# Kernel optimization log

Measured on AMD Instinct MI355X. Metric: run time of the kernel, lower is better.

Reference implementation:

```python
import jax, jax.numpy as jnp
import numpy as np

B, S, H = 2, 2048, 1024
HFF = 4096
E, K = 8, 2

def setup_inputs() -> dict:
    key = jax.random.key(0)
    k1, k2, k3, k4, k5 = jax.random.split(key, 5)
    x = jax.random.normal(k1, (B, S, H), dtype=jnp.float32)
    topk_probs = jax.random.uniform(k2, (B, S, K), dtype=jnp.float32)
    topk_indices = jax.random.randint(k3, (B, S, K), 0, E, dtype=jnp.int64)
    stdv = 1.0 / np.sqrt(H)
    W1 = jax.random.uniform(k4, (E, HFF, H), minval=-stdv, maxval=stdv, dtype=jnp.float32)
    stdv2 = 1.0 / np.sqrt(HFF)
    W2 = jax.random.uniform(k5, (E, H, HFF), minval=-stdv2, maxval=stdv2, dtype=jnp.float32)
    return {"x": x, "topk_probs": topk_probs, "topk_indices": topk_indices, "W1": W1, "W2": W2}

def reference(x, topk_probs, topk_indices, W1, W2):
    # gate[b,s,e] = max_k topk_probs[b,s,k] * (topk_indices[b,s,k]==e)
    # (max over k, matching probs_mask.max(dim=-1) in the torch module)
    e_ids = jnp.arange(E, dtype=topk_indices.dtype)  # [E]
    sel = topk_indices[..., None] == e_ids  # [B,S,K,E]
    gate = jnp.max(jnp.where(sel, topk_probs[..., None], 0.0), axis=2)  # [B,S,E]
    # dense per-expert FFN over all tokens (as the original computes)
    h = jnp.einsum('bsh,efh->ebsf', x, W1)       # [E,B,S,HFF]
    h = jax.nn.gelu(h)
    y = jnp.einsum('ebsf,ehf->ebsh', h, W2)      # [E,B,S,H]
    # probability applied after FFN, masked combine over experts
    out = jnp.einsum('bse,ebsh->bsh', gate, y)   # [B,S,H]
    return out
```

## Files before the change

### kernel.cpp

```cpp
#include <hip/hip_runtime.h>

typedef unsigned short ushort_t;
typedef __attribute__((ext_vector_type(8))) short short8;
typedef __attribute__((ext_vector_type(4))) float f32x4;

#define TOKENS  4096
#define H_DIM   1024
#define HFF_DIM 4096
#define NEXP    8

__device__ __forceinline__ ushort_t f2b(float f) {
    union { float f; unsigned u; } v; v.f = f;
    unsigned r = v.u + 0x7fffu + ((v.u >> 16) & 1u);
    return (ushort_t)(r >> 16);
}

__device__ __forceinline__ float gelu_tanh(float x) {
    float u = 0.7978845608028654f * (x + 0.044715f * x * x * x);
    return 0.5f * x * (1.0f + tanhf(u));
}

__global__ void route_kernel(const float* __restrict__ probs,
                             const int* __restrict__ idx,
                             int* __restrict__ count,
                             int* __restrict__ token_id,
                             float* __restrict__ gate) {
    int t = blockIdx.x * blockDim.x + threadIdx.x;
    if (t >= TOKENS) return;
    int i0 = idx[t * 2 + 0];
    int i1 = idx[t * 2 + 1];
    float p0 = probs[t * 2 + 0];
    float p1 = probs[t * 2 + 1];
    if (i0 == i1) {
        float p = fmaxf(p0, p1);
        int pos = atomicAdd(&count[i0], 1);
        token_id[i0 * TOKENS + pos] = t;
        gate[i0 * TOKENS + pos] = p;
    } else {
        int pos = atomicAdd(&count[i0], 1);
        token_id[i0 * TOKENS + pos] = t;
        gate[i0 * TOKENS + pos] = p0;
        pos = atomicAdd(&count[i1], 1);
        token_id[i1 * TOKENS + pos] = t;
        gate[i1 * TOKENS + pos] = p1;
    }
}

__global__ void prefix_kernel(const int* __restrict__ count, int* __restrict__ offsets) {
    if (threadIdx.x == 0 && blockIdx.x == 0) {
        int acc = 0;
        for (int e = 0; e < NEXP; ++e) { offsets[e] = acc; acc += count[e]; }
        offsets[NEXP] = acc;
    }
}

__global__ __launch_bounds__(256) void gemm1_kernel(
        const float* __restrict__ x, const float* __restrict__ W1,
        const int* __restrict__ count, const int* __restrict__ offsets,
        const int* __restrict__ token_id, ushort_t* __restrict__ h) {
    const int e = blockIdx.z;
    const int cnt = count[e];
    const int mt = blockIdx.y;
    if (mt * 128 >= cnt) return;
    const int nt = blockIdx.x;
    const int base = offsets[e];

    __shared__ __align__(16) ushort_t As[128 * 32];
    __shared__ __align__(16) ushort_t Bs[128 * 32];

    const int tid = threadIdx.x;
    const int srow = tid >> 1;
    const int scol = (tid & 1) << 4;

    int am = mt * 128 + srow;
    int amc = am < cnt ? am : (cnt - 1);
    const int tok = token_id[e * TOKENS + amc];
    const float* aptr = x + (size_t)tok * H_DIM + scol;
    const float* bptr = W1 + (size_t)e * HFF_DIM * H_DIM
                        + (size_t)(nt * 128 + srow) * H_DIM + scol;

    const int lane = tid & 63;
    const int wave = tid >> 6;
    const int wm = (wave >> 1) << 6;
    const int wn = (wave & 1) << 6;
    const int lr = lane & 15;
    const int lq = lane >> 4;

    f32x4 acc[4][4];
#pragma unroll
    for (int mi = 0; mi < 4; ++mi)
#pragma unroll
        for (int ni = 0; ni < 4; ++ni)
            acc[mi][ni] = (f32x4){0.f, 0.f, 0.f, 0.f};

    for (int k0 = 0; k0 < H_DIM; k0 += 32) {
        ushort_t ta[16], tb[16];
        const float4* pa = (const float4*)(aptr + k0);
        const float4* pb = (const float4*)(bptr + k0);
#pragma unroll
        for (int i = 0; i < 4; ++i) {
            float4 va = pa[i];
            ta[i * 4 + 0] = f2b(va.x); ta[i * 4 + 1] = f2b(va.y);
            ta[i * 4 + 2] = f2b(va.z); ta[i * 4 + 3] = f2b(va.w);
            float4 vb = pb[i];
            tb[i * 4 + 0] = f2b(vb.x); tb[i * 4 + 1] = f2b(vb.y);
            tb[i * 4 + 2] = f2b(vb.z); tb[i * 4 + 3] = f2b(vb.w);
        }
        __syncthreads();
        *(short8*)&As[srow * 32 + scol]     = *(short8*)&ta[0];
        *(short8*)&As[srow * 32 + scol + 8] = *(short8*)&ta[8];
        *(short8*)&Bs[srow * 32 + scol]     = *(short8*)&tb[0];
        *(short8*)&Bs[srow * 32 + scol + 8] = *(short8*)&tb[8];
        __syncthreads();

        short8 af[4], bf[4];
#pragma unroll
        for (int mi = 0; mi < 4; ++mi)
            af[mi] = *(const short8*)&As[(wm + mi * 16 + lr) * 32 + lq * 8];
#pragma unroll
        for (int ni = 0; ni < 4; ++ni)
            bf[ni] = *(const short8*)&Bs[(wn + ni * 16 + lr) * 32 + lq * 8];
#pragma unroll
        for (int mi = 0; mi < 4; ++mi)
#pragma unroll
            for (int ni = 0; ni < 4; ++ni)
                acc[mi][ni] = __builtin_amdgcn_mfma_f32_16x16x32_bf16(
                    af[mi], bf[ni], acc[mi][ni], 0, 0, 0);
    }

#pragma unroll
    for (int mi = 0; mi < 4; ++mi) {
#pragma unroll
        for (int r = 0; r < 4; ++r) {
            int m = mt * 128 + wm + mi * 16 + lq * 4 + r;
            if (m < cnt) {
                ushort_t* hp = h + (size_t)(base + m) * HFF_DIM + nt * 128 + wn + lr;
#pragma unroll
                for (int ni = 0; ni < 4; ++ni)
                    hp[ni * 16] = f2b(gelu_tanh(acc[mi][ni][r]));
            }
        }
    }
}

__global__ __launch_bounds__(256) void gemm2_kernel(
        const ushort_t* __restrict__ h, const float* __restrict__ W2,
        const int* __restrict__ count, const int* __restrict__ offsets,
        const int* __restrict__ token_id, const float* __restrict__ gate,
        float* __restrict__ out) {
    const int e = blockIdx.z;
    const int cnt = count[e];
    const int mt = blockIdx.y;
    if (mt * 128 >= cnt) return;
    const int nt = blockIdx.x;
    const int base = offsets[e];

    __shared__ __align__(16) ushort_t As[128 * 32];
    __shared__ __align__(16) ushort_t Bs[128 * 32];

    const int tid = threadIdx.x;
    const int srow = tid >> 1;
    const int scol = (tid & 1) << 4;

    int am = mt * 128 + srow;
    int amc = am < cnt ? am : (cnt - 1);
    const ushort_t* aptr = h + (size_t)(base + amc) * HFF_DIM + scol;
    const float* bptr = W2 + (size_t)e * H_DIM * HFF_DIM
                        + (size_t)(nt * 128 + srow) * HFF_DIM + scol;

    const int lane = tid & 63;
    const int wave = tid >> 6;
    const int wm = (wave >> 1) << 6;
    const int wn = (wave & 1) << 6;
    const int lr = lane & 15;
    const int lq = lane >> 4;

    f32x4 acc[4][4];
#pragma unroll
    for (int mi = 0; mi < 4; ++mi)
#pragma unroll
        for (int ni = 0; ni < 4; ++ni)
            acc[mi][ni] = (f32x4){0.f, 0.f, 0.f, 0.f};

    for (int k0 = 0; k0 < HFF_DIM; k0 += 32) {
        short8 a0 = *(const short8*)(aptr + k0);
        short8 a1 = *(const short8*)(aptr + k0 + 8);
        ushort_t tb[16];
        const float4* pb = (const float4*)(bptr + k0);
#pragma unroll
        for (int i = 0; i < 4; ++i) {
            float4 vb = pb[i];
            tb[i * 4 + 0] = f2b(vb.x); tb[i * 4 + 1] = f2b(vb.y);
            tb[i * 4 + 2] = f2b(vb.z); tb[i * 4 + 3] = f2b(vb.w);
        }
        __syncthreads();
        *(short8*)&As[srow * 32 + scol]     = a0;
        *(short8*)&As[srow * 32 + scol + 8] = a1;
        *(short8*)&Bs[srow * 32 + scol]     = *(short8*)&tb[0];
        *(short8*)&Bs[srow * 32 + scol + 8] = *(short8*)&tb[8];
        __syncthreads();

        short8 af[4], bf[4];
#pragma unroll
        for (int mi = 0; mi < 4; ++mi)
            af[mi] = *(const short8*)&As[(wm + mi * 16 + lr) * 32 + lq * 8];
#pragma unroll
        for (int ni = 0; ni < 4; ++ni)
            bf[ni] = *(const short8*)&Bs[(wn + ni * 16 + lr) * 32 + lq * 8];
#pragma unroll
        for (int mi = 0; mi < 4; ++mi)
#pragma unroll
            for (int ni = 0; ni < 4; ++ni)
                acc[mi][ni] = __builtin_amdgcn_mfma_f32_16x16x32_bf16(
                    af[mi], bf[ni], acc[mi][ni], 0, 0, 0);
    }

#pragma unroll
    for (int mi = 0; mi < 4; ++mi) {
#pragma unroll
        for (int r = 0; r < 4; ++r) {
            int m = mt * 128 + wm + mi * 16 + lq * 4 + r;
            if (m < cnt) {
                int tok = token_id[e * TOKENS + m];
                float g = gate[e * TOKENS + m];
                float* op = out + (size_t)tok * H_DIM + nt * 128 + wn + lr;
#pragma unroll
                for (int ni = 0; ni < 4; ++ni)
                    atomicAdd(&op[ni * 16], g * acc[mi][ni][r]);
            }
        }
    }
}

extern "C" void kernel_launch(void* const* d_in, const int* in_sizes, int n_in,
                              void* d_out, int out_size, void* d_ws, size_t ws_size,
                              hipStream_t stream) {
    const float* x     = (const float*)d_in[0];
    const float* probs = (const float*)d_in[1];
    const int*   idx   = (const int*)d_in[2];
    const float* W1    = (const float*)d_in[3];
    const float* W2    = (const float*)d_in[4];
    float* out = (float*)d_out;

    char* ws = (char*)d_ws;
    int*      count    = (int*)ws;
    int*      offsets  = (int*)(ws + 64);
    int*      token_id = (int*)(ws + 4096);
    float*    gate     = (float*)(ws + 4096 + 8 * 4096 * 4);
    ushort_t* h        = (ushort_t*)(ws + (1 << 20));

    hipMemsetAsync(count, 0, 64, stream);
    hipMemsetAsync(out, 0, (size_t)out_size * sizeof(float), stream);

    route_kernel<<<TOKENS / 256, 256, 0, stream>>>(probs, idx, count, token_id, gate);
    prefix_kernel<<<1, 64, 0, stream>>>(count, offsets);

    dim3 g1(HFF_DIM / 128, TOKENS / 128, NEXP);
    gemm1_kernel<<<g1, 256, 0, stream>>>(x, W1, count, offsets, token_id, h);

    dim3 g2(H_DIM / 128, TOKENS / 128, NEXP);
    gemm2_kernel<<<g2, 256, 0, stream>>>(h, W2, count, offsets, token_id, gate, out);
}
```

Baseline: 654.8 us.

## Pre-cast inputs and weights to bf16 and stage tiles via direct global-to-LDS loads

Adds a cast pass that converts x, W1 and W2 from fp32 to bf16 in workspace. New GEMM kernels then load 16-byte chunks straight into LDS with global_load_lds, removing the per-tile fp32-to-bf16 conversion and register staging. The LDS layout is rearranged so each MFMA operand is one contiguous short8 read. The cost is an extra full read and write of both weight tensors on every call (about 400 MB of traffic). The old path is kept as a fallback when the workspace is too small.

```diff
diff --git a/kernel.cpp b/kernel.cpp
--- a/kernel.cpp
+++ b/kernel.cpp
@@ -1,6 +1,7 @@
 #include <hip/hip_runtime.h>
 
 typedef unsigned short ushort_t;
+typedef __attribute__((ext_vector_type(4))) ushort_t ushort4_t;
 typedef __attribute__((ext_vector_type(8))) short short8;
 typedef __attribute__((ext_vector_type(4))) float f32x4;
 
@@ -18,6 +19,12 @@
 __device__ __forceinline__ float gelu_tanh(float x) {
     float u = 0.7978845608028654f * (x + 0.044715f * x * x * x);
     return 0.5f * x * (1.0f + tanhf(u));
+}
+
+__device__ __forceinline__ void load_lds16(const void* g, void* l) {
+    __builtin_amdgcn_global_load_lds(
+        (const __attribute__((address_space(1))) unsigned int*)g,
+        (__attribute__((address_space(3))) unsigned int*)l, 16, 0, 0);
 }
 
 __global__ void route_kernel(const float* __restrict__ probs,
@@ -54,7 +61,183 @@
     }
 }
 
-__global__ __launch_bounds__(256) void gemm1_kernel(
+__global__ void cast_kernel(const float* __restrict__ in, ushort_t* __restrict__ out, int n4) {
+    int i = blockIdx.x * blockDim.x + threadIdx.x;
+    int stride = gridDim.x * blockDim.x;
+    for (; i < n4; i += stride) {
+        float4 v = ((const float4*)in)[i];
+        ushort4_t o;
+        o.x = f2b(v.x); o.y = f2b(v.y); o.z = f2b(v.z); o.w = f2b(v.w);
+        ((ushort4_t*)out)[i] = o;
+    }
+}
+
+
+__global__ __launch_bounds__(256) void gemm1_fast(
+        const ushort_t* __restrict__ xb, const ushort_t* __restrict__ W1b,
+        const int* __restrict__ count, const int* __restrict__ offsets,
+        const int* __restrict__ token_id, ushort_t* __restrict__ h) {
+    const int e = blockIdx.z;
+    const int cnt = count[e];
+    const int mt = blockIdx.y;
+    if (mt * 128 >= cnt) return;
+    const int nt = blockIdx.x;
+    const int base = offsets[e];
+
+    __shared__ __align__(16) ushort_t As[4096];
+    __shared__ __align__(16) ushort_t Bs[4096];
+
+    const int tid = threadIdx.x;
+    const int row = tid & 127;
+    const int c0 = tid >> 7;
+
+    int am = mt * 128 + row;
+    int amc = am < cnt ? am : (cnt - 1);
+    const int tok = token_id[e * TOKENS + amc];
+    const ushort_t* aptr = xb + (size_t)tok * H_DIM + c0 * 8;
+    const ushort_t* bptr = W1b + (size_t)e * HFF_DIM * H_DIM
+                           + (size_t)(nt * 128 + row) * H_DIM + c0 * 8;
+
+    ushort_t* aL0 = As + tid * 8;
+    ushort_t* aL1 = As + tid * 8 + 2048;
+    ushort_t* bL0 = Bs + tid * 8;
+    ushort_t* bL1 = Bs + tid * 8 + 2048;
+
+    const int lane = tid & 63;
+    const int wave = tid >> 6;
+    const int wm = (wave >> 1) << 6;
+    const int wn = (wave & 1) << 6;
+    const int lr = lane & 15;
+    const int lq = lane >> 4;
+
+    f32x4 acc[4][4];
+#pragma unroll
+    for (int mi = 0; mi < 4; ++mi)
+#pragma unroll
+        for (int ni = 0; ni < 4; ++ni)
+            acc[mi][ni] = (f32x4){0.f, 0.f, 0.f, 0.f};
+
+    for (int k0 = 0; k0 < H_DIM; k0 += 32) {
+        __syncthreads();
+        load_lds16(aptr + k0, aL0);
+        load_lds16(aptr + k0 + 16, aL1);
+        load_lds16(bptr + k0, bL0);
+        load_lds16(bptr + k0 + 16, bL1);
+        __syncthreads();
+
+        short8 af[4], bf[4];
+#pragma unroll
+        for (int mi = 0; mi < 4; ++mi)
+            af[mi] = *(const short8*)&As[(lq * 128 + wm + mi * 16 + lr) * 8];
+#pragma unroll
+        for (int ni = 0; ni < 4; ++ni)
+            bf[ni] = *(const short8*)&Bs[(lq * 128 + wn + ni * 16 + lr) * 8];
+#pragma unroll
+        for (int mi = 0; mi < 4; ++mi)
+#pragma unroll
+            for (int ni = 0; ni < 4; ++ni)
+                acc[mi][ni] = __builtin_amdgcn_mfma_f32_16x16x32_bf16(
+                    af[mi], bf[ni], acc[mi][ni], 0, 0, 0);
+    }
+
+#pragma unroll
+    for (int mi = 0; mi < 4; ++mi) {
+#pragma unroll
+        for (int r = 0; r < 4; ++r) {
+            int m = mt * 128 + wm + mi * 16 + lq * 4 + r;
+            if (m < cnt) {
+                ushort_t* hp = h + (size_t)(base + m) * HFF_DIM + nt * 128 + wn + lr;
+#pragma unroll
+                for (int ni = 0; ni < 4; ++ni)
+                    hp[ni * 16] = f2b(gelu_tanh(acc[mi][ni][r]));
+            }
+        }
+    }
+}
+
+__global__ __launch_bounds__(256) void gemm2_fast(
+        const ushort_t* __restrict__ h, const ushort_t* __restrict__ W2b,
+        const int* __restrict__ count, const int* __restrict__ offsets,
+        const int* __restrict__ token_id, const float* __restrict__ gate,
+        float* __restrict__ out) {
+    const int e = blockIdx.z;
+    const int cnt = count[e];
+    const int mt = blockIdx.y;
+    if (mt * 128 >= cnt) return;
+    const int nt = blockIdx.x;
+    const int base = offsets[e];
+
+    __shared__ __align__(16) ushort_t As[4096];
+    __shared__ __align__(16) ushort_t Bs[4096];
+
+    const int tid = threadIdx.x;
+    const int row = tid & 127;
+    const int c0 = tid >> 7;
+
+    const ushort_t* aptr = h + (size_t)(base + mt * 128 + row) * HFF_DIM + c0 * 8;
+    const ushort_t* bptr = W2b + (size_t)e * H_DIM * HFF_DIM
+                           + (size_t)(nt * 128 + row) * HFF_DIM + c0 * 8;
+
+    ushort_t* aL0 = As + tid * 8;
+    ushort_t* aL1 = As + tid * 8 + 2048;
+    ushort_t* bL0 = Bs + tid * 8;
+    ushort_t* bL1 = Bs + tid * 8 + 2048;
+
+    const int lane = tid & 63;
+    const int wave = tid >> 6;
+    const int wm = (wave >> 1) << 6;
+    const int wn = (wave & 1) << 6;
+    const int lr = lane & 15;
+    const int lq = lane >> 4;
+
+    f32x4 acc[4][4];
+#pragma unroll
+    for (int mi = 0; mi < 4; ++mi)
+#pragma unroll
+        for (int ni = 0; ni < 4; ++ni)
+            acc[mi][ni] = (f32x4){0.f, 0.f, 0.f, 0.f};
+
+    for (int k0 = 0; k0 < HFF_DIM; k0 += 32) {
+        __syncthreads();
+        load_lds16(aptr + k0, aL0);
+        load_lds16(aptr + k0 + 16, aL1);
+        load_lds16(bptr + k0, bL0);
+        load_lds16(bptr + k0 + 16, bL1);
+        __syncthreads();
+
+        short8 af[4], bf[4];
+#pragma unroll
+        for (int mi = 0; mi < 4; ++mi)
+            af[mi] = *(const short8*)&As[(lq * 128 + wm + mi * 16 + lr) * 8];
+#pragma unroll
+        for (int ni = 0; ni < 4; ++ni)
+            bf[ni] = *(const short8*)&Bs[(lq * 128 + wn + ni * 16 + lr) * 8];
+#pragma unroll
+        for (int mi = 0; mi < 4; ++mi)
+#pragma unroll
+            for (int ni = 0; ni < 4; ++ni)
+                acc[mi][ni] = __builtin_amdgcn_mfma_f32_16x16x32_bf16(
+                    af[mi], bf[ni], acc[mi][ni], 0, 0, 0);
+    }
+
+#pragma unroll
+    for (int mi = 0; mi < 4; ++mi) {
+#pragma unroll
+        for (int r = 0; r < 4; ++r) {
+            int m = mt * 128 + wm + mi * 16 + lq * 4 + r;
+            if (m < cnt) {
+                int tok = token_id[e * TOKENS + m];
+                float g = gate[e * TOKENS + m];
+                float* op = out + (size_t)tok * H_DIM + nt * 128 + wn + lr;
+#pragma unroll
+                for (int ni = 0; ni < 4; ++ni)
+                    atomicAdd(&op[ni * 16], g * acc[mi][ni][r]);
+            }
+        }
+    }
+}
+
+__global__ __launch_bounds__(256) void gemm1_slow(
         const float* __restrict__ x, const float* __restrict__ W1,
         const int* __restrict__ count, const int* __restrict__ offsets,
         const int* __restrict__ token_id, ushort_t* __restrict__ h) {
@@ -143,7 +326,7 @@
     }
 }
 
-__global__ __launch_bounds__(256) void gemm2_kernel(
+__global__ __launch_bounds__(256) void gemm2_slow(
         const ushort_t* __restrict__ h, const float* __restrict__ W2,
         const int* __restrict__ count, const int* __restrict__ offsets,
         const int* __restrict__ token_id, const float* __restrict__ gate,
@@ -243,11 +426,16 @@
     float* out = (float*)d_out;
 
     char* ws = (char*)d_ws;
-    int*      count    = (int*)ws;
-    int*      offsets  = (int*)(ws + 64);
-    int*      token_id = (int*)(ws + 4096);
-    float*    gate     = (float*)(ws + 4096 + 8 * 4096 * 4);
-    ushort_t* h        = (ushort_t*)(ws + (1 << 20));
+    int*   count    = (int*)ws;
+    int*   offsets  = (int*)(ws + 64);
+    int*   token_id = (int*)(ws + 4096);
+    float* gate     = (float*)(ws + 4096 + 8 * 4096 * 4);
+
+    const size_t XB_OFF  = 1ull << 20;
+    const size_t W1B_OFF = 16ull << 20;
+    const size_t W2B_OFF = 84ull << 20;
+    const size_t H_OFF   = 156ull << 20;
+    const size_t NEED    = H_OFF + (size_t)(8192 + 128) * HFF_DIM * 2;
 
     hipMemsetAsync(count, 0, 64, stream);
     hipMemsetAsync(out, 0, (size_t)out_size * sizeof(float), stream);
@@ -255,9 +443,28 @@
     route_kernel<<<TOKENS / 256, 256, 0, stream>>>(probs, idx, count, token_id, gate);
     prefix_kernel<<<1, 64, 0, stream>>>(count, offsets);
 
-    dim3 g1(HFF_DIM / 128, TOKENS / 128, NEXP);
-    gemm1_kernel<<<g1, 256, 0, stream>>>(x, W1, count, offsets, token_id, h);
-
-    dim3 g2(H_DIM / 128, TOKENS / 128, NEXP);
-    gemm2_kernel<<<g2, 256, 0, stream>>>(h, W2, count, offsets, token_id, gate, out);
-}
+    if (ws_size >= NEED) {
+        ushort_t* xb  = (ushort_t*)(ws + XB_OFF);
+        ushort_t* W1b = (ushort_t*)(ws + W1B_OFF);
+        ushort_t* W2b = (ushort_t*)(ws + W2B_OFF);
+        ushort_t* h   = (ushort_t*)(ws + H_OFF);
+
+        cast_kernel<<<2048, 256, 0, stream>>>(x, xb, TOKENS * H_DIM / 4);
+        cast_kernel<<<2048, 256, 0, stream>>>(W1, W1b, NEXP * HFF_DIM * H_DIM / 4);
+        cast_kernel<<<2048, 256, 0, stream>>>(W2, W2b, NEXP * H_DIM * HFF_DIM / 4);
+
+        dim3 g1(HFF_DIM / 128, TOKENS / 128, NEXP);
+        gemm1_fast<<<g1, 256, 0, stream>>>(xb, W1b, count, offsets, token_id, h);
+
+        dim3 g2(H_DIM / 128, TOKENS / 128, NEXP);
+        gemm2_fast<<<g2, 256, 0, stream>>>(h, W2b, count, offsets, token_id, gate, out);
+    } else {
+        ushort_t* h = (ushort_t*)(ws + (1 << 20));
+
+        dim3 g1(HFF_DIM / 128, TOKENS / 128, NEXP);
+        gemm1_slow<<<g1, 256, 0, stream>>>(x, W1, count, offsets, token_id, h);
+
+        dim3 g2(H_DIM / 128, TOKENS / 128, NEXP);
+        gemm2_slow<<<g2, 256, 0, stream>>>(h, W2, count, offsets, token_id, gate, out);
+    }
+}
```

New measurement: 767.2 us. 17.2% more time.

## Pre-cast inputs to bf16, prefetch registers, split-K gemm2, repack LDS layout

Applied to the files above, without the earlier changes.

Adds a kernel that converts x, W1 and W2 to bf16 once per call, so the GEMMs load half the bytes and skip per-tile conversion. Both GEMMs now prefetch the next K tile into registers while the current one computes, and use a k-chunk-major LDS layout. gemm2 splits K four ways, giving more blocks at the cost of more atomic adds on the output. The cast pass reads and writes about 268MB of weights every call, which is a large extra memory cost. gemm2 also drops the row clamp, so the last tile reads padded rows past the token count.

```diff
diff --git a/kernel.cpp b/kernel.cpp
--- a/kernel.cpp
+++ b/kernel.cpp
@@ -1,6 +1,7 @@
 #include <hip/hip_runtime.h>
 
 typedef unsigned short ushort_t;
+typedef __attribute__((ext_vector_type(4))) ushort_t ushort4_t;
 typedef __attribute__((ext_vector_type(8))) short short8;
 typedef __attribute__((ext_vector_type(4))) float f32x4;
 
@@ -54,8 +55,29 @@
     }
 }
 
-__global__ __launch_bounds__(256) void gemm1_kernel(
-        const float* __restrict__ x, const float* __restrict__ W1,
+__global__ void cast3_kernel(const float* __restrict__ x, ushort_t* __restrict__ xb,
+                             const float* __restrict__ W1, ushort_t* __restrict__ W1b,
+                             const float* __restrict__ W2, ushort_t* __restrict__ W2b) {
+    const int NX = TOKENS * H_DIM / 4;
+    const int NW = NEXP * HFF_DIM * H_DIM / 4;
+    const int total = NX + 2 * NW;
+    int i = blockIdx.x * blockDim.x + threadIdx.x;
+    int stride = gridDim.x * blockDim.x;
+    for (; i < total; i += stride) {
+        const float4* src; ushort4_t* dst; int j;
+        if (i < NX)           { src = (const float4*)x;  dst = (ushort4_t*)xb;  j = i; }
+        else if (i < NX + NW) { src = (const float4*)W1; dst = (ushort4_t*)W1b; j = i - NX; }
+        else                  { src = (const float4*)W2; dst = (ushort4_t*)W2b; j = i - NX - NW; }
+        float4 v = src[j];
+        ushort4_t o;
+        o.x = f2b(v.x); o.y = f2b(v.y); o.z = f2b(v.z); o.w = f2b(v.w);
+        dst[j] = o;
+    }
+}
+
+
+__global__ __launch_bounds__(256) void gemm1_fast(
+        const ushort_t* __restrict__ xb, const ushort_t* __restrict__ W1b,
         const int* __restrict__ count, const int* __restrict__ offsets,
         const int* __restrict__ token_id, ushort_t* __restrict__ h) {
     const int e = blockIdx.z;
@@ -65,19 +87,24 @@
     const int nt = blockIdx.x;
     const int base = offsets[e];
 
-    __shared__ __align__(16) ushort_t As[128 * 32];
-    __shared__ __align__(16) ushort_t Bs[128 * 32];
+    __shared__ __align__(16) ushort_t As[4096];
+    __shared__ __align__(16) ushort_t Bs[4096];
 
     const int tid = threadIdx.x;
-    const int srow = tid >> 1;
-    const int scol = (tid & 1) << 4;
-
-    int am = mt * 128 + srow;
+    const int row = tid & 127;
+    const int c0 = tid >> 7;
+
+    int am = mt * 128 + row;
     int amc = am < cnt ? am : (cnt - 1);
     const int tok = token_id[e * TOKENS + amc];
-    const float* aptr = x + (size_t)tok * H_DIM + scol;
-    const float* bptr = W1 + (size_t)e * HFF_DIM * H_DIM
-                        + (size_t)(nt * 128 + srow) * H_DIM + scol;
+    const ushort_t* aptr = xb + (size_t)tok * H_DIM + c0 * 8;
+    const ushort_t* bptr = W1b + (size_t)e * HFF_DIM * H_DIM
+                           + (size_t)(nt * 128 + row) * H_DIM + c0 * 8;
+
+    ushort_t* aL0 = As + tid * 8;
+    ushort_t* aL1 = As + tid * 8 + 2048;
+    ushort_t* bL0 = Bs + tid * 8;
+    ushort_t* bL1 = Bs + tid * 8 + 2048;
 
     const int lane = tid & 63;
     const int wave = tid >> 6;
@@ -93,33 +120,33 @@
         for (int ni = 0; ni < 4; ++ni)
             acc[mi][ni] = (f32x4){0.f, 0.f, 0.f, 0.f};
 
+    short8 ra0 = *(const short8*)(aptr);
+    short8 ra1 = *(const short8*)(aptr + 16);
+    short8 rb0 = *(const short8*)(bptr);
+    short8 rb1 = *(const short8*)(bptr + 16);
+
     for (int k0 = 0; k0 < H_DIM; k0 += 32) {
-        ushort_t ta[16], tb[16];
-        const float4* pa = (const float4*)(aptr + k0);
-        const float4* pb = (const float4*)(bptr + k0);
-#pragma unroll
-        for (int i = 0; i < 4; ++i) {
-            float4 va = pa[i];
-            ta[i * 4 + 0] = f2b(va.x); ta[i * 4 + 1] = f2b(va.y);
-            ta[i * 4 + 2] = f2b(va.z); ta[i * 4 + 3] = f2b(va.w);
-            float4 vb = pb[i];
-            tb[i * 4 + 0] = f2b(vb.x); tb[i * 4 + 1] = f2b(vb.y);
-            tb[i * 4 + 2] = f2b(vb.z); tb[i * 4 + 3] = f2b(vb.w);
+        __syncthreads();
+        *(short8*)aL0 = ra0;
+        *(short8*)aL1 = ra1;
+        *(short8*)bL0 = rb0;
+        *(short8*)bL1 = rb1;
+        __syncthreads();
+
+        if (k0 + 32 < H_DIM) {
+            ra0 = *(const short8*)(aptr + k0 + 32);
+            ra1 = *(const short8*)(aptr + k0 + 48);
+            rb0 = *(const short8*)(bptr + k0 + 32);
+            rb1 = *(const short8*)(bptr + k0 + 48);
         }
-        __syncthreads();
-        *(short8*)&As[srow * 32 + scol]     = *(short8*)&ta[0];
-        *(short8*)&As[srow * 32 + scol + 8] = *(short8*)&ta[8];
-        *(short8*)&Bs[srow * 32 + scol]     = *(short8*)&tb[0];
-        *(short8*)&Bs[srow * 32 + scol + 8] = *(short8*)&tb[8];
-        __syncthreads();
 
         short8 af[4], bf[4];
 #pragma unroll
         for (int mi = 0; mi < 4; ++mi)
-            af[mi] = *(const short8*)&As[(wm + mi * 16 + lr) * 32 + lq * 8];
+            af[mi] = *(const short8*)&As[(lq * 128 + wm + mi * 16 + lr) * 8];
 #pragma unroll
         for (int ni = 0; ni < 4; ++ni)
-            bf[ni] = *(const short8*)&Bs[(wn + ni * 16 + lr) * 32 + lq * 8];
+            bf[ni] = *(const short8*)&Bs[(lq * 128 + wn + ni * 16 + lr) * 8];
 #pragma unroll
         for (int mi = 0; mi < 4; ++mi)
 #pragma unroll
@@ -143,30 +170,36 @@
     }
 }
 
-__global__ __launch_bounds__(256) void gemm2_kernel(
-        const ushort_t* __restrict__ h, const float* __restrict__ W2,
+__global__ __launch_bounds__(256) void gemm2_fast(
+        const ushort_t* __restrict__ h, const ushort_t* __restrict__ W2b,
         const int* __restrict__ count, const int* __restrict__ offsets,
         const int* __restrict__ token_id, const float* __restrict__ gate,
         float* __restrict__ out) {
-    const int e = blockIdx.z;
+    const int e = blockIdx.z >> 2;
+    const int kz = blockIdx.z & 3;
     const int cnt = count[e];
     const int mt = blockIdx.y;
     if (mt * 128 >= cnt) return;
     const int nt = blockIdx.x;
     const int base = offsets[e];
-
-    __shared__ __align__(16) ushort_t As[128 * 32];
-    __shared__ __align__(16) ushort_t Bs[128 * 32];
+    const int kbeg = kz * (HFF_DIM / 4);
+    const int kend = kbeg + (HFF_DIM / 4);
+
+    __shared__ __align__(16) ushort_t As[4096];
+    __shared__ __align__(16) ushort_t Bs[4096];
 
     const int tid = threadIdx.x;
-    const int srow = tid >> 1;
-    const int scol = (tid & 1) << 4;
-
-    int am = mt * 128 + srow;
-    int amc = am < cnt ? am : (cnt - 1);
-    const ushort_t* aptr = h + (size_t)(base + amc) * HFF_DIM + scol;
-    const float* bptr = W2 + (size_t)e * H_DIM * HFF_DIM
-                        + (size_t)(nt * 128 + srow) * HFF_DIM + scol;
+    const int row = tid & 127;
+    const int c0 = tid >> 7;
+
+    const ushort_t* aptr = h + (size_t)(base + mt * 128 + row) * HFF_DIM + c0 * 8;
+    const ushort_t* bptr = W2b + (size_t)e * H_DIM * HFF_DIM
+                           + (size_t)(nt * 128 + row) * HFF_DIM + c0 * 8;
+
+    ushort_t* aL0 = As + tid * 8;
+    ushort_t* aL1 = As + tid * 8 + 2048;
+    ushort_t* bL0 = Bs + tid * 8;
+    ushort_t* bL1 = Bs + tid * 8 + 2048;
 
     const int lane = tid & 63;
     const int wave = tid >> 6;
@@ -182,31 +215,33 @@
         for (int ni = 0; ni < 4; ++ni)
             acc[mi][ni] = (f32x4){0.f, 0.f, 0.f, 0.f};
 
-    for (int k0 = 0; k0 < HFF_DIM; k0 += 32) {
-        short8 a0 = *(const short8*)(aptr + k0);
-        short8 a1 = *(const short8*)(aptr + k0 + 8);
-        ushort_t tb[16];
-        const float4* pb = (const float4*)(bptr + k0);
-#pragma unroll
-        for (int i = 0; i < 4; ++i) {
-            float4 vb = pb[i];
-            tb[i * 4 + 0] = f2b(vb.x); tb[i * 4 + 1] = f2b(vb.y);
-            tb[i * 4 + 2] = f2b(vb.z); tb[i * 4 + 3] = f2b(vb.w);
+    short8 ra0 = *(const short8*)(aptr + kbeg);
+    short8 ra1 = *(const short8*)(aptr + kbeg + 16);
+    short8 rb0 = *(const short8*)(bptr + kbeg);
+    short8 rb1 = *(const short8*)(bptr + kbeg + 16);
+
+    for (int k0 = kbeg; k0 < kend; k0 += 32) {
+        __syncthreads();
+        *(short8*)aL0 = ra0;
+        *(short8*)aL1 = ra1;
+        *(short8*)bL0 = rb0;
+        *(short8*)bL1 = rb1;
+        __syncthreads();
+
+        if (k0 + 32 < kend) {
+            ra0 = *(const short8*)(aptr + k0 + 32);
+            ra1 = *(const short8*)(aptr + k0 + 48);
+            rb0 = *(const short8*)(bptr + k0 + 32);
+            rb1 = *(const short8*)(bptr + k0 + 48);
         }
-        __syncthreads();
-        *(short8*)&As[srow * 32 + scol]     = a0;
-        *(short8*)&As[srow * 32 + scol + 8] = a1;
-        *(short8*)&Bs[srow * 32 + scol]     = *(short8*)&tb[0];
-        *(short8*)&Bs[srow * 32 + scol + 8] = *(short8*)&tb[8];
-        __syncthreads();
 
         short8 af[4], bf[4];
 #pragma unroll
         for (int mi = 0; mi < 4; ++mi)
-            af[mi] = *(const short8*)&As[(wm + mi * 16 + lr) * 32 + lq * 8];
+            af[mi] = *(const short8*)&As[(lq * 128 + wm + mi * 16 + lr) * 8];
 #pragma unroll
         for (int ni = 0; ni < 4; ++ni)
-            bf[ni] = *(const short8*)&Bs[(wn + ni * 16 + lr) * 32 + lq * 8];
+            bf[ni] = *(const short8*)&Bs[(lq * 128 + wn + ni * 16 + lr) * 8];
 #pragma unroll
         for (int mi = 0; mi < 4; ++mi)
 #pragma unroll
@@ -243,11 +278,20 @@
     float* out = (float*)d_out;
 
     char* ws = (char*)d_ws;
-    int*      count    = (int*)ws;
-    int*      offsets  = (int*)(ws + 64);
-    int*      token_id = (int*)(ws + 4096);
-    float*    gate     = (float*)(ws + 4096 + 8 * 4096 * 4);
-    ushort_t* h        = (ushort_t*)(ws + (1 << 20));
+    int*   count    = (int*)ws;
+    int*   offsets  = (int*)(ws + 64);
+    int*   token_id = (int*)(ws + 4096);
+    float* gate     = (float*)(ws + 4096 + 8 * 4096 * 4);
+
+    const size_t XB_OFF  = 1ull << 20;
+    const size_t W1B_OFF = 16ull << 20;
+    const size_t W2B_OFF = 84ull << 20;
+    const size_t H_OFF   = 156ull << 20;
+
+    ushort_t* xb  = (ushort_t*)(ws + XB_OFF);
+    ushort_t* W1b = (ushort_t*)(ws + W1B_OFF);
+    ushort_t* W2b = (ushort_t*)(ws + W2B_OFF);
+    ushort_t* h   = (ushort_t*)(ws + H_OFF);
 
     hipMemsetAsync(count, 0, 64, stream);
     hipMemsetAsync(out, 0, (size_t)out_size * sizeof(float), stream);
@@ -255,9 +299,11 @@
     route_kernel<<<TOKENS / 256, 256, 0, stream>>>(probs, idx, count, token_id, gate);
     prefix_kernel<<<1, 64, 0, stream>>>(count, offsets);
 
+    cast3_kernel<<<4096, 256, 0, stream>>>(x, xb, W1, W1b, W2, W2b);
+
     dim3 g1(HFF_DIM / 128, TOKENS / 128, NEXP);
-    gemm1_kernel<<<g1, 256, 0, stream>>>(x, W1, count, offsets, token_id, h);
-
-    dim3 g2(H_DIM / 128, TOKENS / 128, NEXP);
-    gemm2_kernel<<<g2, 256, 0, stream>>>(h, W2, count, offsets, token_id, gate, out);
-}
+    gemm1_fast<<<g1, 256, 0, stream>>>(xb, W1b, count, offsets, token_id, h);
+
+    dim3 g2(H_DIM / 128, TOKENS / 128, NEXP * 4);
+    gemm2_fast<<<g2, 256, 0, stream>>>(h, W2b, count, offsets, token_id, gate, out);
+}
```

After: 725.8 us. 1.11x slower.
